# Kernel optimization log

Hardware: AMD Instinct MI355X
Metric: run time of the kernel (lower is better)

## Reference

```python
import jax, jax.numpy as jnp
import numpy as np

NUM_RELATION = 7

def setup_inputs() -> dict:
    key = jax.random.key(0)
    ks = jax.random.split(key, 12)
    N, E, D, DO, R, DE = 20000, 640000, 512, 512, NUM_RELATION, 59
    inp = {
        "node_feat": jax.random.normal(ks[0], (N, D), dtype=jnp.float32),
        "edge_weight": jax.random.uniform(ks[1], (E,), dtype=jnp.float32),
        "edge_feat": jax.random.normal(ks[2], (E, DE), dtype=jnp.float32),
        "W_lin": jax.random.normal(ks[3], (DO, R * D), dtype=jnp.float32) * 0.02,
        "b_lin": jax.random.normal(ks[4], (DO,), dtype=jnp.float32) * 0.02,
        "W_self": jax.random.normal(ks[5], (DO, D), dtype=jnp.float32) * 0.02,
        "b_self": jax.random.normal(ks[6], (DO,), dtype=jnp.float32) * 0.02,
        "W_edge": jax.random.normal(ks[7], (DO, DE), dtype=jnp.float32) * 0.02,
        "b_edge": jax.random.normal(ks[8], (DO,), dtype=jnp.float32) * 0.02,
        "node_in": jax.random.randint(ks[9], (E,), 0, N, dtype=jnp.int64) if jax.config.jax_enable_x64 else jax.random.randint(ks[9], (E,), 0, N).astype(jnp.int32),
        "node_out": jax.random.randint(ks[10], (E,), 0, N).astype(jnp.int32),
        "relation": jax.random.randint(ks[11], (E,), 0, R).astype(jnp.int32),
    }
    inp["node_in"] = inp["node_in"].astype(jnp.int32)
    return inp


def reference(node_feat, edge_weight, edge_feat, W_lin, b_lin, W_self, b_self,
              W_edge, b_edge, node_in, node_out, relation):
    N, D = node_feat.shape
    R = NUM_RELATION
    # segment id: node_out * R + relation  (column index in sparse (N, N*R) adjacency)
    seg = node_out * R + relation  # [E]
    # update = adjacency.T @ input  == scatter-add of weighted source features
    msg = node_feat[node_in] * edge_weight[:, None]               # [E, D]
    update = jax.ops.segment_sum(msg, seg, num_segments=N * R)    # [N*R, D]
    # edge_linear path: edge_update scattered with the same segment ids
    edge_msg = (edge_feat @ W_edge.T + b_edge) * edge_weight[:, None]  # [E, D]
    update = update + jax.ops.segment_sum(edge_msg, seg, num_segments=N * R)
    update = update.reshape(N, R * D)                             # [N, R*D]
    # combine: linear(update) + self_loop(input), then relu
    out = update @ W_lin.T + b_lin + node_feat @ W_self.T + b_self
    return jax.nn.relu(out)
```

## Files before the change

### kernel.cpp

```cpp
#include <hip/hip_runtime.h>
#include <stdint.h>

typedef unsigned short u16;
typedef __attribute__((ext_vector_type(8))) __bf16 bf16x8;
typedef __attribute__((ext_vector_type(8))) unsigned short u16x8;
typedef __attribute__((ext_vector_type(4))) float f32x4;

#define NREL 7
#define DIM  512
#define DEDGE 59
#define KC   420
#define KCP  448
#define KU   3584
#define KTOT 4544

__device__ __forceinline__ float bf2f(u16 u) {
  union { unsigned u; float f; } c; c.u = ((unsigned)u) << 16; return c.f;
}
__device__ __forceinline__ u16 f2bf(float f) {
  union { float f; unsigned u; } c; c.f = f;
  unsigned r = ((c.u >> 16) & 1u) + 0x7FFFu;
  return (u16)((c.u + r) >> 16);
}

__device__ __forceinline__ void gload16(const void* g, void* l) {
  __builtin_amdgcn_global_load_lds(
      (__attribute__((address_space(1))) void*)g,
      (__attribute__((address_space(3))) void*)l, 16, 0, 0);
}

__global__ void convA(const float* __restrict__ in, u16* __restrict__ out, int total4) {
  int i = blockIdx.x * 256 + threadIdx.x;
  if (i >= total4) return;
  float4 v = ((const float4*)in)[i];
  ushort4 r;
  r.x = f2bf(v.x); r.y = f2bf(v.y); r.z = f2bf(v.z); r.w = f2bf(v.w);
  ((ushort4*)out)[i] = r;
}

__global__ void buildBW(const float* __restrict__ W_lin, const float* __restrict__ W_self,
                        u16* __restrict__ Bfull, int total4) {
  int gid = blockIdx.x * 256 + threadIdx.x;
  if (gid >= total4) return;
  int idx = gid * 4;
  int o = idx >> 12;
  int k = idx & 4095;
  const float* src = (k < KU) ? (W_lin + (size_t)o * KU + k)
                              : (W_self + (size_t)o * DIM + (k - KU));
  float4 v = *(const float4*)src;
  ushort4 rr;
  rr.x = f2bf(v.x); rr.y = f2bf(v.y); rr.z = f2bf(v.z); rr.w = f2bf(v.w);
  *(ushort4*)(Bfull + (size_t)o * KTOT + k) = rr;
}

__global__ __launch_bounds__(512) void buildCx(const float* __restrict__ W_edge,
                                               const float* __restrict__ b_edge,
                                               const float* __restrict__ W_lin,
                                               u16* __restrict__ Bfull) {
  int c = blockIdx.x;
  int o = threadIdx.x;
  u16* dst = Bfull + (size_t)o * KTOT + KU + DIM;
  if (c >= KC) { dst[c] = 0; return; }
  __shared__ float col[DIM];
  int r;
  if (c < NREL * DEDGE) {
    r = c / DEDGE;
    int de = c - r * DEDGE;
    col[o] = W_edge[(size_t)o * DEDGE + de];
  } else {
    r = c - NREL * DEDGE;
    col[o] = b_edge[o];
  }
  __syncthreads();
  const float4* wv = (const float4*)(W_lin + (size_t)o * KU + (size_t)r * DIM);
  float acc = 0.f;
#pragma unroll 4
  for (int d4 = 0; d4 < DIM / 4; ++d4) {
    float4 wq = wv[d4];
    acc += col[d4 * 4 + 0] * wq.x + col[d4 * 4 + 1] * wq.y
         + col[d4 * 4 + 2] * wq.z + col[d4 * 4 + 3] * wq.w;
  }
  dst[c] = f2bf(acc);
}

__global__ void countK2(const int* __restrict__ node_out, const int* __restrict__ relation,
                        int* __restrict__ counts2, int E) {
  int e = blockIdx.x * 256 + threadIdx.x;
  if (e < E) atomicAdd(&counts2[node_out[e] * 8 + relation[e]], 1);
}

__global__ void baseK(const int* __restrict__ counts2, int* __restrict__ offs2,
                      int* __restrict__ cursor2, int* __restrict__ totalCtr, int N) {
  int n = blockIdx.x * 256 + threadIdx.x;
  if (n >= N) return;
  int cnt[NREL];
  int s = 0;
#pragma unroll
  for (int r = 0; r < NREL; ++r) { cnt[r] = counts2[n * 8 + r]; s += cnt[r]; }
  int base = atomicAdd(totalCtr, s);
#pragma unroll
  for (int r = 0; r < NREL; ++r) {
    offs2[n * 8 + r] = base;
    cursor2[n * 8 + r] = base;
    base += cnt[r];
  }
  offs2[n * 8 + 7] = base;
}

__global__ void fillK2(const int* __restrict__ node_in, const int* __restrict__ node_out,
                       const int* __restrict__ relation, const float* __restrict__ ew,
                       int* __restrict__ cursor2, uint4* __restrict__ quads, int E) {
  int e = blockIdx.x * 256 + threadIdx.x;
  if (e >= E) return;
  int p = atomicAdd(&cursor2[node_out[e] * 8 + relation[e]], 1);
  quads[p] = make_uint4((unsigned)node_in[e], __float_as_uint(ew[e]), (unsigned)e, 0u);
}

__global__ __launch_bounds__(64) void gatherG2(const float* __restrict__ ef,
                                               const uint4* __restrict__ quads,
                                               const int* __restrict__ offs2,
                                               u16* __restrict__ G) {
  int n = blockIdx.x;
  int lane = threadIdx.x;
  u16* grow = G + (size_t)n * KCP;
  int base = n * 8;
  for (int r = 0; r < NREL; ++r) {
    int p0 = offs2[base + r], p1 = offs2[base + r + 1];
    float acc = 0.f;
    for (int p = p0; p < p1; ++p) {
      uint4 q = quads[p];
      int e = __builtin_amdgcn_readfirstlane((int)q.z);
      float w = __uint_as_float(__builtin_amdgcn_readfirstlane(q.y));
      float v = (lane < DEDGE) ? ef[(size_t)e * DEDGE + lane] : 1.0f;
      acc += w * v;
    }
    if (lane < DEDGE) grow[r * DEDGE + lane] = f2bf(acc);
    else if (lane == DEDGE) grow[NREL * DEDGE + r] = f2bf(acc);
  }
  if (lane >= 60) {
    for (int c = KC + (lane - 60); c < KCP; c += 4) grow[c] = 0;
  }
}

__global__ __launch_bounds__(256) void aggK(const u16* __restrict__ NF,
                                            const uint4* __restrict__ quads,
                                            const int* __restrict__ offs2,
                                            u16* __restrict__ U) {
  int n = blockIdx.x;
  int wid = threadIdx.x >> 6, lane = threadIdx.x & 63;
  int o0 = lane * 8;
  u16* urow = U + (size_t)n * KU;
  int base = n * 8;
  for (int r = wid; r < NREL; r += 4) {
    int p0 = offs2[base + r], p1 = offs2[base + r + 1];
    float a[8];
#pragma unroll
    for (int j = 0; j < 8; ++j) a[j] = 0.f;
    for (int p = p0; p < p1; ++p) {
      uint4 q = quads[p];
      int src = __builtin_amdgcn_readfirstlane((int)q.x);
      float w = __uint_as_float(__builtin_amdgcn_readfirstlane(q.y));
      u16x8 hv = *(const u16x8*)(NF + (size_t)src * DIM + o0);
#pragma unroll
      for (int j = 0; j < 8; ++j) a[j] += w * bf2f(hv[j]);
    }
    u16x8 st;
#pragma unroll
    for (int j = 0; j < 8; ++j) st[j] = f2bf(a[j]);
    *(u16x8*)(urow + (size_t)r * DIM + o0) = st;
  }
}

__global__ __launch_bounds__(256) void gemm_br(const u16* __restrict__ U,
                                               const u16* __restrict__ NF,
                                               const u16* __restrict__ G,
                                               const u16* __restrict__ Bt,
                                               const float* __restrict__ b_lin,
                                               const float* __restrict__ b_self,
                                               float* __restrict__ Cout, int M) {
  __shared__ __align__(16) u16 sA[3][128 * 32];
  __shared__ __align__(16) u16 sB[3][128 * 32];
  const int tid = threadIdx.x;
  const int w = tid >> 6, l = tid & 63;
  const int lr = l & 15, kg = l >> 4;
  const int sl = kg ^ ((lr >> 1) & 3);

  const int id = blockIdx.x;
  const int npan = gridDim.x >> 2;
  const int nfull = (npan >> 3) << 3;
  int p, c;
  if (id < nfull * 4) {
    int g = id >> 5, r = id & 31;
    p = g * 8 + (r & 7);
    c = r >> 3;
  } else {
    int t = id - nfull * 4;
    p = nfull + (t >> 2);
    c = t & 3;
  }
  const int m0 = p * 128, n0 = c * 128;
  const int wr = w >> 1, wc = w & 1;
  f32x4 acc[4][4];
  const f32x4 z4 = {0.f, 0.f, 0.f, 0.f};
#pragma unroll
  for (int i = 0; i < 4; ++i)
#pragma unroll
    for (int j = 0; j < 4; ++j) acc[i][j] = z4;

  const int ktiles = KTOT / 32;

  auto stage = [&](int kt, int b) {
    const u16* Ab; int astr, ac0;
    if (kt < 112)      { Ab = U;  astr = KU;  ac0 = kt * 32; }
    else if (kt < 128) { Ab = NF; astr = DIM; ac0 = kt * 32 - KU; }
    else               { Ab = G;  astr = KCP; ac0 = kt * 32 - (KU + DIM); }
    const int k0 = kt * 32;
#pragma unroll
    for (int t = 0; t < 2; ++t) {
      int idx = w * 128 + t * 64 + l;
      int row = idx >> 2, kp = idx & 3;
      int s = kp ^ ((row >> 1) & 3);
      int gm = m0 + row; gm = gm < M ? gm : M - 1;
      gload16(Ab + (size_t)gm * astr + ac0 + s * 8,
              (char*)sA[b] + (size_t)idx * 16);
    }
#pragma unroll
    for (int t = 0; t < 2; ++t) {
      int idx = w * 128 + t * 64 + l;
      int row = idx >> 2, kp = idx & 3;
      int s = kp ^ ((row >> 1) & 3);
      gload16(Bt + (size_t)(n0 + row) * KTOT + k0 + s * 8,
              (char*)sB[b] + (size_t)idx * 16);
    }
  };

  stage(0, 0);
  stage(1, 1);
  asm volatile("s_waitcnt vmcnt(4)" ::: "memory");
  __builtin_amdgcn_s_barrier();
  __builtin_amdgcn_sched_barrier(0);

  for (int kt = 0; kt < ktiles; ++kt) {
    const int cur = kt % 3;
    if (kt + 2 < ktiles) stage(kt + 2, (kt + 2) % 3);
    bf16x8 af[4], bfr[4];
#pragma unroll
    for (int i = 0; i < 4; ++i)
      af[i] = *(const bf16x8*)(sA[cur] + (size_t)(wr * 64 + i * 16 + lr) * 32 + sl * 8);
#pragma unroll
    for (int j = 0; j < 4; ++j)
      bfr[j] = *(const bf16x8*)(sB[cur] + (size_t)(wc * 64 + j * 16 + lr) * 32 + sl * 8);
#pragma unroll
    for (int i = 0; i < 4; ++i)
#pragma unroll
      for (int j = 0; j < 4; ++j)
        acc[i][j] = __builtin_amdgcn_mfma_f32_16x16x32_bf16(af[i], bfr[j], acc[i][j], 0, 0, 0);
    if (kt + 2 < ktiles) {
      asm volatile("s_waitcnt vmcnt(4)" ::: "memory");
    } else {
      asm volatile("s_waitcnt vmcnt(0)" ::: "memory");
    }
    __builtin_amdgcn_s_barrier();
    __builtin_amdgcn_sched_barrier(0);
  }
#pragma unroll
  for (int i = 0; i < 4; ++i) {
#pragma unroll
    for (int j = 0; j < 4; ++j) {
      int gj = n0 + wc * 64 + j * 16 + lr;
      float bias = b_lin[gj] + b_self[gj];
#pragma unroll
      for (int v = 0; v < 4; ++v) {
        int gm = m0 + wr * 64 + i * 16 + kg * 4 + v;
        if (gm < M)
          ((float*)Cout)[(size_t)gm * DIM + gj] = fmaxf(acc[i][j][v] + bias, 0.f);
      }
    }
  }
}

extern "C" void kernel_launch(void* const* d_in, const int* in_sizes, int n_in,
                              void* d_out, int out_size, void* d_ws, size_t ws_size,
                              hipStream_t stream) {
  const float* node_feat = (const float*)d_in[0];
  const float* edge_weight = (const float*)d_in[1];
  const float* edge_feat = (const float*)d_in[2];
  const float* W_lin = (const float*)d_in[3];
  const float* b_lin = (const float*)d_in[4];
  const float* W_self = (const float*)d_in[5];
  const float* b_self = (const float*)d_in[6];
  const float* W_edge = (const float*)d_in[7];
  const float* b_edge = (const float*)d_in[8];
  const int* node_in = (const int*)d_in[9];
  const int* node_out = (const int*)d_in[10];
  const int* relation = (const int*)d_in[11];
  float* out = (float*)d_out;

  const int N = in_sizes[0] / DIM;
  const int E = in_sizes[1];

  char* ws = (char*)d_ws;
  size_t off = 0;
  auto take = [&](size_t b) {
    char* p = ws + off;
    off += (b + 255) & ~(size_t)255;
    return p;
  };
  u16* NF       = (u16*)take((size_t)N * DIM * 2);
  u16* Bfull    = (u16*)take((size_t)DIM * KTOT * 2);
  u16* U        = (u16*)take((size_t)N * KU * 2);
  u16* G        = (u16*)take((size_t)N * KCP * 2);
  int* counts2  = (int*)take((size_t)N * 8 * 4);
  int* offs2    = (int*)take((size_t)N * 8 * 4);
  int* cursor2  = (int*)take((size_t)N * 8 * 4);
  int* totalCtr = (int*)take(256);
  uint4* quads  = (uint4*)take((size_t)E * 16);
  if (off > ws_size) return;

  hipMemsetAsync(counts2, 0, (size_t)N * 8 * 4, stream);
  hipMemsetAsync(totalCtr, 0, 256, stream);

  {
    int total4 = N * DIM / 4;
    convA<<<(total4 + 255) / 256, 256, 0, stream>>>(node_feat, NF, total4);
  }
  {
    int total4 = DIM * 4096 / 4;
    buildBW<<<(total4 + 255) / 256, 256, 0, stream>>>(W_lin, W_self, Bfull, total4);
  }
  buildCx<<<KCP, 512, 0, stream>>>(W_edge, b_edge, W_lin, Bfull);

  countK2<<<(E + 255) / 256, 256, 0, stream>>>(node_out, relation, counts2, E);
  baseK<<<(N + 255) / 256, 256, 0, stream>>>(counts2, offs2, cursor2, totalCtr, N);
  fillK2<<<(E + 255) / 256, 256, 0, stream>>>(node_in, node_out, relation, edge_weight,
                                              cursor2, quads, E);

  gatherG2<<<N, 64, 0, stream>>>(edge_feat, quads, offs2, G);
  aggK<<<N, 256, 0, stream>>>(NF, quads, offs2, U);

  {
    int npan = (N + 127) / 128;
    gemm_br<<<npan * 4, 256, 0, stream>>>(U, NF, G, Bfull, b_lin, b_self, out, N);
  }
}
```

Before: 475.4 us.

## Fuse prep kernels into one launch and batch edge-weight folding by eight columns

Merges node-feature conversion, weight conversion, the edge count pass and padding zeroing into a single multi-role kernel, which removes several launches and lets the independent work overlap. The edge-weight folding kernel now computes eight columns per block, so each W_lin row is read 56 times instead of 420. The trade-off is fewer blocks (56) for that step, which could leave the GPU under-occupied, and more register pressure from eight accumulators per thread.

Measured after the change: 454.8 us (median of 2 runs). 1.05x faster.

```diff
diff --git a/kernel.cpp b/kernel.cpp
--- a/kernel.cpp
+++ b/kernel.cpp
@@ -29,64 +29,87 @@
       (__attribute__((address_space(3))) void*)l, 16, 0, 0);
 }
 
-__global__ void convA(const float* __restrict__ in, u16* __restrict__ out, int total4) {
-  int i = blockIdx.x * 256 + threadIdx.x;
-  if (i >= total4) return;
-  float4 v = ((const float4*)in)[i];
-  ushort4 r;
-  r.x = f2bf(v.x); r.y = f2bf(v.y); r.z = f2bf(v.z); r.w = f2bf(v.w);
-  ((ushort4*)out)[i] = r;
-}
-
-__global__ void buildBW(const float* __restrict__ W_lin, const float* __restrict__ W_self,
-                        u16* __restrict__ Bfull, int total4) {
-  int gid = blockIdx.x * 256 + threadIdx.x;
-  if (gid >= total4) return;
-  int idx = gid * 4;
-  int o = idx >> 12;
-  int k = idx & 4095;
-  const float* src = (k < KU) ? (W_lin + (size_t)o * KU + k)
-                              : (W_self + (size_t)o * DIM + (k - KU));
-  float4 v = *(const float4*)src;
-  ushort4 rr;
-  rr.x = f2bf(v.x); rr.y = f2bf(v.y); rr.z = f2bf(v.z); rr.w = f2bf(v.w);
-  *(ushort4*)(Bfull + (size_t)o * KTOT + k) = rr;
-}
-
-__global__ __launch_bounds__(512) void buildCx(const float* __restrict__ W_edge,
-                                               const float* __restrict__ b_edge,
-                                               const float* __restrict__ W_lin,
-                                               u16* __restrict__ Bfull) {
-  int c = blockIdx.x;
+__global__ __launch_bounds__(256) void prep1(const float* __restrict__ nf_in,
+                                             u16* __restrict__ NF,
+                                             const float* __restrict__ W_lin,
+                                             const float* __restrict__ W_self,
+                                             u16* __restrict__ Bfull,
+                                             const int* __restrict__ node_out,
+                                             const int* __restrict__ relation,
+                                             int* __restrict__ counts2,
+                                             int totalA4, int bA, int bB, int bC, int E) {
+  int bid = blockIdx.x;
+  int t = threadIdx.x;
+  if (bid < bA) {
+    int i = bid * 256 + t;
+    if (i >= totalA4) return;
+    float4 v = ((const float4*)nf_in)[i];
+    ushort4 r;
+    r.x = f2bf(v.x); r.y = f2bf(v.y); r.z = f2bf(v.z); r.w = f2bf(v.w);
+    ((ushort4*)NF)[i] = r;
+  } else if (bid < bB) {
+    int gid = (bid - bA) * 256 + t;
+    int idx = gid * 4;
+    int o = idx >> 12;
+    int k = idx & 4095;
+    const float* src = (k < KU) ? (W_lin + (size_t)o * KU + k)
+                                : (W_self + (size_t)o * DIM + (k - KU));
+    float4 v = *(const float4*)src;
+    ushort4 rr;
+    rr.x = f2bf(v.x); rr.y = f2bf(v.y); rr.z = f2bf(v.z); rr.w = f2bf(v.w);
+    *(ushort4*)(Bfull + (size_t)o * KTOT + k) = rr;
+  } else if (bid < bC) {
+    int e = (bid - bB) * 256 + t;
+    if (e < E) atomicAdd(&counts2[node_out[e] * 8 + relation[e]], 1);
+  } else {
+    int idx = (bid - bC) * 256 + t;
+    if (idx < DIM * (KCP - KC)) {
+      int o = idx / (KCP - KC), c = idx - o * (KCP - KC);
+      Bfull[(size_t)o * KTOT + KU + DIM + KC + c] = 0;
+    }
+  }
+}
+
+__global__ __launch_bounds__(512) void buildCx8(const float* __restrict__ W_edge,
+                                                const float* __restrict__ b_edge,
+                                                const float* __restrict__ W_lin,
+                                                u16* __restrict__ Bfull) {
+  __shared__ __align__(16) float cols[DIM][8];
+  int r = blockIdx.x >> 3, chunk = blockIdx.x & 7;
   int o = threadIdx.x;
-  u16* dst = Bfull + (size_t)o * KTOT + KU + DIM;
-  if (c >= KC) { dst[c] = 0; return; }
-  __shared__ float col[DIM];
-  int r;
-  if (c < NREL * DEDGE) {
-    r = c / DEDGE;
-    int de = c - r * DEDGE;
-    col[o] = W_edge[(size_t)o * DEDGE + de];
-  } else {
-    r = c - NREL * DEDGE;
-    col[o] = b_edge[o];
+#pragma unroll
+  for (int s = 0; s < 8; ++s) {
+    int de = chunk * 8 + s;
+    float v = 0.f;
+    if (de < DEDGE) v = W_edge[(size_t)o * DEDGE + de];
+    else if (de == DEDGE) v = b_edge[o];
+    cols[o][s] = v;
   }
   __syncthreads();
   const float4* wv = (const float4*)(W_lin + (size_t)o * KU + (size_t)r * DIM);
-  float acc = 0.f;
-#pragma unroll 4
+  float acc[8];
+#pragma unroll
+  for (int s = 0; s < 8; ++s) acc[s] = 0.f;
   for (int d4 = 0; d4 < DIM / 4; ++d4) {
     float4 wq = wv[d4];
-    acc += col[d4 * 4 + 0] * wq.x + col[d4 * 4 + 1] * wq.y
-         + col[d4 * 4 + 2] * wq.z + col[d4 * 4 + 3] * wq.w;
-  }
-  dst[c] = f2bf(acc);
-}
-
-__global__ void countK2(const int* __restrict__ node_out, const int* __restrict__ relation,
-                        int* __restrict__ counts2, int E) {
-  int e = blockIdx.x * 256 + threadIdx.x;
-  if (e < E) atomicAdd(&counts2[node_out[e] * 8 + relation[e]], 1);
+#pragma unroll
+    for (int dd = 0; dd < 4; ++dd) {
+      float wqd = (dd == 0) ? wq.x : (dd == 1) ? wq.y : (dd == 2) ? wq.z : wq.w;
+      const float4* cp = (const float4*)&cols[d4 * 4 + dd][0];
+      float4 c0 = cp[0], c1 = cp[1];
+      acc[0] += wqd * c0.x; acc[1] += wqd * c0.y;
+      acc[2] += wqd * c0.z; acc[3] += wqd * c0.w;
+      acc[4] += wqd * c1.x; acc[5] += wqd * c1.y;
+      acc[6] += wqd * c1.z; acc[7] += wqd * c1.w;
+    }
+  }
+  u16* dst = Bfull + (size_t)o * KTOT + KU + DIM;
+#pragma unroll
+  for (int s = 0; s < 8; ++s) {
+    int de = chunk * 8 + s;
+    if (de < DEDGE) dst[(size_t)r * DEDGE + de] = f2bf(acc[s]);
+    else if (de == DEDGE) dst[NREL * DEDGE + r] = f2bf(acc[s]);
+  }
 }
 
 __global__ void baseK(const int* __restrict__ counts2, int* __restrict__ offs2,
@@ -321,16 +344,17 @@
   hipMemsetAsync(totalCtr, 0, 256, stream);
 
   {
-    int total4 = N * DIM / 4;
-    convA<<<(total4 + 255) / 256, 256, 0, stream>>>(node_feat, NF, total4);
-  }
-  {
-    int total4 = DIM * 4096 / 4;
-    buildBW<<<(total4 + 255) / 256, 256, 0, stream>>>(W_lin, W_self, Bfull, total4);
-  }
-  buildCx<<<KCP, 512, 0, stream>>>(W_edge, b_edge, W_lin, Bfull);
-
-  countK2<<<(E + 255) / 256, 256, 0, stream>>>(node_out, relation, counts2, E);
+    int totalA4 = N * DIM / 4;
+    int bA = (totalA4 + 255) / 256;
+    int bB = bA + (DIM * 4096 / 4) / 256;
+    int bC = bB + (E + 255) / 256;
+    int bD = bC + (DIM * (KCP - KC) + 255) / 256;
+    prep1<<<bD, 256, 0, stream>>>(node_feat, NF, W_lin, W_self, Bfull,
+                                  node_out, relation, counts2,
+                                  totalA4, bA, bB, bC, E);
+  }
+  buildCx8<<<NREL * 8, 512, 0, stream>>>(W_edge, b_edge, W_lin, Bfull);
+
   baseK<<<(N + 255) / 256, 256, 0, stream>>>(counts2, offs2, cursor2, totalCtr, N);
   fillK2<<<(E + 255) / 256, 256, 0, stream>>>(node_in, node_out, relation, edge_weight,
                                               cursor2, quads, E);
```
